# Kernel optimization log

Hardware: AMD Instinct MI355X
Metric: run time of the kernel (lower is better)

The kernel has to match this reference:

```python
import jax, jax.numpy as jnp
import numpy as np
from jax import lax

HIDDEN = 30
NUM_CLASSES = 10
SEQ = 784
BATCH = 16384


def setup_inputs() -> dict:
    key = jax.random.key(0)
    k = jax.random.split(key, 6)
    s_ih = 1.0  # fan_in = 1
    s_hh = 1.0 / np.sqrt(HIDDEN)
    s_lin = 1.0 / np.sqrt(HIDDEN)
    return {
        "inputs": jax.random.normal(k[0], (BATCH, SEQ), dtype=jnp.float32),
        "W_ih": jax.random.normal(k[1], (HIDDEN, 1), dtype=jnp.float32) * s_ih,
        "W_hh": jax.random.normal(k[2], (HIDDEN, HIDDEN), dtype=jnp.float32) * s_hh,
        "b_mod": jax.random.normal(k[3], (HIDDEN,), dtype=jnp.float32) * 0.1,
        "W_lin": jax.random.normal(k[4], (NUM_CLASSES, HIDDEN), dtype=jnp.float32) * s_lin,
        "b_lin": jax.random.normal(k[5], (NUM_CLASSES,), dtype=jnp.float32) * s_lin,
    }


def reference(inputs, W_ih, W_hh, b_mod, W_lin, b_lin):
    # inputs: [B, 784] pixel-by-pixel sequence. Scan over the 784 time steps.
    B = inputs.shape[0]
    # Precompute the input projection for all steps at once: [784, B, H]
    # (W_ih has shape [H, 1], so x_t @ W_ih.T == x_t[:, None] * W_ih[:, 0])
    x_proj = inputs.T[:, :, None] * W_ih[:, 0][None, None, :]  # [784, B, H]

    def step(h, xp):
        z = xp + h @ W_hh.T  # [B, H]
        # modReLU: sign(z) * relu(|z| + b)
        h_new = jnp.sign(z) * jax.nn.relu(jnp.abs(z) + b_mod)
        return h_new, None

    h0 = jnp.zeros((B, HIDDEN), dtype=inputs.dtype)
    h_final, _ = lax.scan(step, h0, x_proj)
    return h_final @ W_lin.T + b_lin  # [B, 10] logits
```

## Files before the change

kernel.cpp:

```cpp
#include <hip/hip_runtime.h>
#include <stdint.h>

#define HID 30
#define NCLS 10
#define SEQ 784
#define NBATCH 16384
#define TCH 112
#define NSTAGE 7
#define XPAD 116

typedef _Float16 f16x8 __attribute__((ext_vector_type(8)));
typedef _Float16 f16x2 __attribute__((ext_vector_type(2)));
typedef float f32x4 __attribute__((ext_vector_type(4)));
typedef uint32_t u32x4 __attribute__((ext_vector_type(4)));

static __device__ __forceinline__ f16x8 mkfrag16(uint32_t a, uint32_t b, uint32_t c, uint32_t d) {
    u32x4 t = {a, b, c, d};
    return __builtin_bit_cast(f16x8, t);
}

static __device__ __forceinline__ uint32_t pkf16(_Float16 lo, _Float16 hi) {
    return (uint32_t)__builtin_bit_cast(unsigned short, lo)
         | ((uint32_t)__builtin_bit_cast(unsigned short, hi) << 16);
}

static __device__ __forceinline__ uint32_t pk_rne(float a, float b) {
    return pkf16((_Float16)a, (_Float16)b);
}

static __device__ __forceinline__ uint32_t pkrtz(float a, float b) {
    return __builtin_bit_cast(uint32_t, __builtin_amdgcn_cvt_pkrtz(a, b));
}

static __device__ __forceinline__ uint32_t modrelu_pk(uint32_t z, uint32_t bp) {
    const f16x2 zero2 = {(_Float16)0.f, (_Float16)0.f};
    f16x2 t = __builtin_bit_cast(f16x2, z & 0x7FFF7FFFu) + __builtin_bit_cast(f16x2, bp);
    t = __builtin_elementwise_max(t, zero2);
    const uint32_t tb = __builtin_bit_cast(uint32_t, t);
    return (tb & 0x7FFF7FFFu) | (z & 0x80008000u);
}

static __device__ __forceinline__ uint32_t pkmax(uint32_t a, uint32_t b) {
    return __builtin_bit_cast(uint32_t,
        __builtin_elementwise_max(__builtin_bit_cast(f16x2, a), __builtin_bit_cast(f16x2, b)));
}

static __device__ __forceinline__ uint32_t scale_mul(uint32_t v, uint32_t sc32) {
    return __builtin_bit_cast(uint32_t,
        __builtin_bit_cast(f16x2, v) * __builtin_bit_cast(f16x2, sc32));
}

__launch_bounds__(64, 1)
__global__ void rnn_scan_kernel(const float* __restrict__ inp,
                                const float* __restrict__ W_ih,
                                const float* __restrict__ W_hh,
                                const float* __restrict__ b_mod,
                                const float* __restrict__ W_lin,
                                const float* __restrict__ b_lin,
                                float* __restrict__ out)
{
    __shared__ __align__(16) float xs_lds[16 * XPAD];

    const int lane = threadIdx.x;
    const int q = lane >> 4;
    const int n = lane & 15;
    const int b0 = blockIdx.x * 16;

    const int i1 = 8 * (n >> 2) + (n & 3);
    const int i2 = i1 + 4;

    uint32_t a1h[4], a1m[4], a2h[4], a2m[4];
    #pragma unroll
    for (int p = 0; p < 4; ++p) {
        _Float16 h1[2], m1[2], h2[2], m2[2];
        #pragma unroll
        for (int e = 0; e < 2; ++e) {
            const int j = 8 * q + 2 * p + e;
            float w1 = 0.f, w2 = 0.f;
            if (j < HID) {
                w1 = W_hh[i1 * HID + j];
                if (i2 < HID) w2 = W_hh[i2 * HID + j];
            } else if (j == HID) {
                w1 = W_ih[i1];
                if (i2 < HID) w2 = W_ih[i2];
            }
            h1[e] = (_Float16)w1; m1[e] = (_Float16)(w1 - (float)h1[e]);
            h2[e] = (_Float16)w2; m2[e] = (_Float16)(w2 - (float)h2[e]);
        }
        a1h[p] = pkf16(h1[0], h1[1]); a1m[p] = pkf16(m1[0], m1[1]);
        a2h[p] = pkf16(h2[0], h2[1]); a2m[p] = pkf16(m2[0], m2[1]);
    }
    const f16x8 A1h = mkfrag16(a1h[0], a1h[1], a1h[2], a1h[3]);
    const f16x8 A1m = mkfrag16(a1m[0], a1m[1], a1m[2], a1m[3]);
    const f16x8 A2h = mkfrag16(a2h[0], a2h[1], a2h[2], a2h[3]);
    const f16x8 A2m = mkfrag16(a2m[0], a2m[1], a2m[2], a2m[3]);

    uint32_t bSp[4];
    #pragma unroll
    for (int p = 0; p < 4; ++p) {
        const int ja = 8 * q + 2 * p;
        const int jb = ja + 1;
        const float ba = (ja < HID) ? b_mod[ja] : 0.f;
        const float bb = (jb < HID) ? b_mod[jb] : 0.f;
        bSp[p] = pk_rne(ba, bb);
    }

    uint32_t hp[4] = {0u, 0u, 0u, 0u};
    int xinv_e = 0;
    int pend_field = 15;

    const bool isq3 = (q == 3);
    const f32x4 z4 = {0.f, 0.f, 0.f, 0.f};

    auto do8 = [&](const uint32_t* xpk) {
        #pragma unroll
        for (int tt = 0; tt < 8; ++tt) {
            const f16x8 Bh = mkfrag16(hp[0], hp[1], hp[2], hp[3]);
            f32x4 d1 = __builtin_amdgcn_mfma_f32_16x16x32_f16(A1h, Bh, z4, 0, 0, 0);
            f32x4 d2 = __builtin_amdgcn_mfma_f32_16x16x32_f16(A2h, Bh, z4, 0, 0, 0);
            d1 = __builtin_amdgcn_mfma_f32_16x16x32_f16(A1m, Bh, d1, 0, 0, 0);
            d2 = __builtin_amdgcn_mfma_f32_16x16x32_f16(A2m, Bh, d2, 0, 0, 0);
            hp[0] = modrelu_pk(pk_rne(d1[0], d1[1]), bSp[0]);
            hp[1] = modrelu_pk(pk_rne(d1[2], d1[3]), bSp[1]);
            hp[2] = modrelu_pk(pk_rne(d2[0], d2[1]), bSp[2]);
            const uint32_t mr3 = modrelu_pk(pk_rne(d2[2], d2[3]), bSp[3]);
            hp[3] = isq3 ? xpk[(tt + 1) & 7] : mr3;
        }
    };

    for (int s = 0; s < NSTAGE; ++s) {
        #pragma unroll
        for (int r = 0; r < 7; ++r) {
            const int idx = r * 64 + lane;
            const int bl = idx / 28;
            const int t4 = idx % 28;
            const float4 v = *(const float4*)(inp + (size_t)(b0 + bl) * SEQ + s * TCH + t4 * 4);
            *(float4*)(&xs_lds[bl * XPAD + t4 * 4]) = v;
        }
        __syncthreads();

        const float* xrow = &xs_lds[n * XPAD];
        float4 xv0 = *(const float4*)(xrow);
        float4 xv1 = *(const float4*)(xrow + 4);

        for (int t16 = 0; t16 < 7; ++t16) {
            const uint32_t sc32 = (uint32_t)pend_field * 0x04000400u;
            #pragma unroll
            for (int p = 0; p < 4; ++p) hp[p] = scale_mul(hp[p], sc32);
            #pragma unroll
            for (int p = 0; p < 4; ++p) bSp[p] = scale_mul(bSp[p], sc32);
            xinv_e += pend_field - 15;

            const float fac = __uint_as_float((uint32_t)(127 + xinv_e) << 23);

            {
                const int toff = t16 * 16 + 8;
                const float4 xn0 = *(const float4*)(xrow + toff);
                const float4 xn1 = *(const float4*)(xrow + toff + 4);

                uint32_t xpk[8];
                xpk[0] = pkrtz(xv0.x * fac, 0.f); xpk[1] = pkrtz(xv0.y * fac, 0.f);
                xpk[2] = pkrtz(xv0.z * fac, 0.f); xpk[3] = pkrtz(xv0.w * fac, 0.f);
                xpk[4] = pkrtz(xv1.x * fac, 0.f); xpk[5] = pkrtz(xv1.y * fac, 0.f);
                xpk[6] = pkrtz(xv1.z * fac, 0.f); xpk[7] = pkrtz(xv1.w * fac, 0.f);
                hp[3] = isq3 ? xpk[0] : hp[3];

                {
                    uint32_t mx = pkmax(pkmax(hp[0] & 0x7FFF7FFFu, hp[1] & 0x7FFF7FFFu),
                                        pkmax(hp[2] & 0x7FFF7FFFu, hp[3] & 0x7FFF7FFFu));
                    mx = pkmax(mx, (uint32_t)__shfl_xor((int)mx, 16));
                    mx = pkmax(mx, (uint32_t)__shfl_xor((int)mx, 32));
                    const uint32_t e16 = max(mx & 0xFFFFu, mx >> 16);
                    const int e_raw = (int)(e16 >> 10);
                    pend_field = min(max(25 - e_raw, 1), 20);
                }

                do8(xpk);
                xv0 = xn0;
                xv1 = xn1;
            }

            {
                const int toff = (t16 < 6) ? (t16 + 1) * 16 : 0;
                const float4 xn0 = *(const float4*)(xrow + toff);
                const float4 xn1 = *(const float4*)(xrow + toff + 4);

                uint32_t xpk[8];
                xpk[0] = pkrtz(xv0.x * fac, 0.f); xpk[1] = pkrtz(xv0.y * fac, 0.f);
                xpk[2] = pkrtz(xv0.z * fac, 0.f); xpk[3] = pkrtz(xv0.w * fac, 0.f);
                xpk[4] = pkrtz(xv1.x * fac, 0.f); xpk[5] = pkrtz(xv1.y * fac, 0.f);
                xpk[6] = pkrtz(xv1.z * fac, 0.f); xpk[7] = pkrtz(xv1.w * fac, 0.f);
                hp[3] = isq3 ? xpk[0] : hp[3];

                do8(xpk);
                xv0 = xn0;
                xv1 = xn1;
            }
        }
        __syncthreads();
    }

    const float S = __uint_as_float((uint32_t)(127 - xinv_e) << 23);
    float hf[8];
    #pragma unroll
    for (int p = 0; p < 4; ++p) {
        const f16x2 v = __builtin_bit_cast(f16x2, hp[p]);
        hf[2 * p] = (float)v.x;
        hf[2 * p + 1] = (float)v.y;
    }
    float acc[NCLS];
    #pragma unroll
    for (int c = 0; c < NCLS; ++c) {
        float p = 0.f;
        #pragma unroll
        for (int k = 0; k < 8; ++k) {
            const int j = 8 * q + k;
            if (j < HID) p += W_lin[c * HID + j] * hf[k];
        }
        p += __shfl_xor(p, 16, 64);
        p += __shfl_xor(p, 32, 64);
        acc[c] = p * S + b_lin[c];
    }
    if (q == 0) {
        #pragma unroll
        for (int c = 0; c < NCLS; ++c)
            out[(size_t)(b0 + n) * NCLS + c] = acc[c];
    }
}

extern "C" void kernel_launch(void* const* d_in, const int* in_sizes, int n_in,
                              void* d_out, int out_size, void* d_ws, size_t ws_size,
                              hipStream_t stream) {
    const float* inp   = (const float*)d_in[0];
    const float* W_ih  = (const float*)d_in[1];
    const float* W_hh  = (const float*)d_in[2];
    const float* b_mod = (const float*)d_in[3];
    const float* W_lin = (const float*)d_in[4];
    const float* b_lin = (const float*)d_in[5];
    float* out = (float*)d_out;

    dim3 grid(NBATCH / 16);
    dim3 block(64);
    hipLaunchKernelGGL(rnn_scan_kernel, grid, block, 0, stream,
                       inp, W_ih, W_hh, b_mod, W_lin, b_lin, out);
}
```

Before: 181.8 us.

## Interleave two independent batch chains per wave and overlap exponent reductions

Each 64-thread block now carries two independent 16-sample recurrent chains (A and B). Their MFMA and modReLU steps are interleaved so one chain's dependent work can fill the other's MFMA latency. The cross-lane max shuffles used for dynamic rescaling are split and issued around the MFMA steps to hide their latency, and the grid is halved accordingly. The trade-off is twice the registers and LDS per block and only half as many waves, so some SIMDs may sit idle with 512 single-wave blocks.

```diff
diff --git a/kernel.cpp b/kernel.cpp
--- a/kernel.cpp
+++ b/kernel.cpp
@@ -20,8 +20,8 @@
 }
 
 static __device__ __forceinline__ uint32_t pkf16(_Float16 lo, _Float16 hi) {
-    return (uint32_t)__builtin_bit_cast(unsigned short, lo)
-         | ((uint32_t)__builtin_bit_cast(unsigned short, hi) << 16);
+    f16x2 v = {lo, hi};
+    return __builtin_bit_cast(uint32_t, v);
 }
 
 static __device__ __forceinline__ uint32_t pk_rne(float a, float b) {
@@ -59,12 +59,12 @@
                                 const float* __restrict__ b_lin,
                                 float* __restrict__ out)
 {
-    __shared__ __align__(16) float xs_lds[16 * XPAD];
+    __shared__ __align__(16) float xs_lds[32 * XPAD];
 
     const int lane = threadIdx.x;
     const int q = lane >> 4;
     const int n = lane & 15;
-    const int b0 = blockIdx.x * 16;
+    const int b0 = blockIdx.x * 32;
 
     const int i1 = 8 * (n >> 2) + (n & 3);
     const int i2 = i1 + 4;
@@ -95,42 +95,57 @@
     const f16x8 A2h = mkfrag16(a2h[0], a2h[1], a2h[2], a2h[3]);
     const f16x8 A2m = mkfrag16(a2m[0], a2m[1], a2m[2], a2m[3]);
 
-    uint32_t bSp[4];
+    uint32_t bSpA[4], bSpB[4];
     #pragma unroll
     for (int p = 0; p < 4; ++p) {
         const int ja = 8 * q + 2 * p;
         const int jb = ja + 1;
         const float ba = (ja < HID) ? b_mod[ja] : 0.f;
         const float bb = (jb < HID) ? b_mod[jb] : 0.f;
-        bSp[p] = pk_rne(ba, bb);
-    }
-
-    uint32_t hp[4] = {0u, 0u, 0u, 0u};
-    int xinv_e = 0;
-    int pend_field = 15;
+        const uint32_t v = pk_rne(ba, bb);
+        bSpA[p] = v;
+        bSpB[p] = v;
+    }
+
+    uint32_t hpA[4] = {0u, 0u, 0u, 0u};
+    uint32_t hpB[4] = {0u, 0u, 0u, 0u};
+    int xinvA = 0, xinvB = 0;
+    int pendA = 15, pendB = 15;
 
     const bool isq3 = (q == 3);
     const f32x4 z4 = {0.f, 0.f, 0.f, 0.f};
 
-    auto do8 = [&](const uint32_t* xpk) {
+    auto do8x2 = [&](const uint32_t* xa, const uint32_t* xb) {
         #pragma unroll
         for (int tt = 0; tt < 8; ++tt) {
-            const f16x8 Bh = mkfrag16(hp[0], hp[1], hp[2], hp[3]);
-            f32x4 d1 = __builtin_amdgcn_mfma_f32_16x16x32_f16(A1h, Bh, z4, 0, 0, 0);
-            f32x4 d2 = __builtin_amdgcn_mfma_f32_16x16x32_f16(A2h, Bh, z4, 0, 0, 0);
-            d1 = __builtin_amdgcn_mfma_f32_16x16x32_f16(A1m, Bh, d1, 0, 0, 0);
-            d2 = __builtin_amdgcn_mfma_f32_16x16x32_f16(A2m, Bh, d2, 0, 0, 0);
-            hp[0] = modrelu_pk(pk_rne(d1[0], d1[1]), bSp[0]);
-            hp[1] = modrelu_pk(pk_rne(d1[2], d1[3]), bSp[1]);
-            hp[2] = modrelu_pk(pk_rne(d2[0], d2[1]), bSp[2]);
-            const uint32_t mr3 = modrelu_pk(pk_rne(d2[2], d2[3]), bSp[3]);
-            hp[3] = isq3 ? xpk[(tt + 1) & 7] : mr3;
+            const f16x8 BA = mkfrag16(hpA[0], hpA[1], hpA[2], hpA[3]);
+            const f16x8 BB = mkfrag16(hpB[0], hpB[1], hpB[2], hpB[3]);
+            f32x4 d1A = __builtin_amdgcn_mfma_f32_16x16x32_f16(A1h, BA, z4, 0, 0, 0);
+            f32x4 d2A = __builtin_amdgcn_mfma_f32_16x16x32_f16(A2h, BA, z4, 0, 0, 0);
+            f32x4 d1B = __builtin_amdgcn_mfma_f32_16x16x32_f16(A1h, BB, z4, 0, 0, 0);
+            f32x4 d2B = __builtin_amdgcn_mfma_f32_16x16x32_f16(A2h, BB, z4, 0, 0, 0);
+            d1A = __builtin_amdgcn_mfma_f32_16x16x32_f16(A1m, BA, d1A, 0, 0, 0);
+            d2A = __builtin_amdgcn_mfma_f32_16x16x32_f16(A2m, BA, d2A, 0, 0, 0);
+            d1B = __builtin_amdgcn_mfma_f32_16x16x32_f16(A1m, BB, d1B, 0, 0, 0);
+            d2B = __builtin_amdgcn_mfma_f32_16x16x32_f16(A2m, BB, d2B, 0, 0, 0);
+
+            hpA[0] = modrelu_pk(pk_rne(d1A[0], d1A[1]), bSpA[0]);
+            hpA[1] = modrelu_pk(pk_rne(d1A[2], d1A[3]), bSpA[1]);
+            hpA[2] = modrelu_pk(pk_rne(d2A[0], d2A[1]), bSpA[2]);
+            const uint32_t mr3A = modrelu_pk(pk_rne(d2A[2], d2A[3]), bSpA[3]);
+            hpA[3] = isq3 ? xa[(tt + 1) & 7] : mr3A;
+
+            hpB[0] = modrelu_pk(pk_rne(d1B[0], d1B[1]), bSpB[0]);
+            hpB[1] = modrelu_pk(pk_rne(d1B[2], d1B[3]), bSpB[1]);
+            hpB[2] = modrelu_pk(pk_rne(d2B[0], d2B[1]), bSpB[2]);
+            const uint32_t mr3B = modrelu_pk(pk_rne(d2B[2], d2B[3]), bSpB[3]);
+            hpB[3] = isq3 ? xb[(tt + 1) & 7] : mr3B;
         }
     };
 
     for (int s = 0; s < NSTAGE; ++s) {
         #pragma unroll
-        for (int r = 0; r < 7; ++r) {
+        for (int r = 0; r < 14; ++r) {
             const int idx = r * 64 + lane;
             const int bl = idx / 28;
             const int t4 = idx % 28;
@@ -139,92 +154,133 @@
         }
         __syncthreads();
 
-        const float* xrow = &xs_lds[n * XPAD];
-        float4 xv0 = *(const float4*)(xrow);
-        float4 xv1 = *(const float4*)(xrow + 4);
+        const float* xrowA = &xs_lds[n * XPAD];
+        const float* xrowB = &xs_lds[(16 + n) * XPAD];
+        float4 xvA0 = *(const float4*)(xrowA);
+        float4 xvA1 = *(const float4*)(xrowA + 4);
+        float4 xvB0 = *(const float4*)(xrowB);
+        float4 xvB1 = *(const float4*)(xrowB + 4);
 
         for (int t16 = 0; t16 < 7; ++t16) {
-            const uint32_t sc32 = (uint32_t)pend_field * 0x04000400u;
+            const uint32_t scA = (uint32_t)pendA * 0x04000400u;
+            const uint32_t scB = (uint32_t)pendB * 0x04000400u;
             #pragma unroll
-            for (int p = 0; p < 4; ++p) hp[p] = scale_mul(hp[p], sc32);
+            for (int p = 0; p < 4; ++p) { hpA[p] = scale_mul(hpA[p], scA); hpB[p] = scale_mul(hpB[p], scB); }
             #pragma unroll
-            for (int p = 0; p < 4; ++p) bSp[p] = scale_mul(bSp[p], sc32);
-            xinv_e += pend_field - 15;
-
-            const float fac = __uint_as_float((uint32_t)(127 + xinv_e) << 23);
+            for (int p = 0; p < 4; ++p) { bSpA[p] = scale_mul(bSpA[p], scA); bSpB[p] = scale_mul(bSpB[p], scB); }
+            xinvA += pendA - 15;
+            xinvB += pendB - 15;
+
+            const float facA = __uint_as_float((uint32_t)(127 + xinvA) << 23);
+            const float facB = __uint_as_float((uint32_t)(127 + xinvB) << 23);
+
+            uint32_t mxA, mxB;
 
             {
                 const int toff = t16 * 16 + 8;
-                const float4 xn0 = *(const float4*)(xrow + toff);
-                const float4 xn1 = *(const float4*)(xrow + toff + 4);
-
-                uint32_t xpk[8];
-                xpk[0] = pkrtz(xv0.x * fac, 0.f); xpk[1] = pkrtz(xv0.y * fac, 0.f);
-                xpk[2] = pkrtz(xv0.z * fac, 0.f); xpk[3] = pkrtz(xv0.w * fac, 0.f);
-                xpk[4] = pkrtz(xv1.x * fac, 0.f); xpk[5] = pkrtz(xv1.y * fac, 0.f);
-                xpk[6] = pkrtz(xv1.z * fac, 0.f); xpk[7] = pkrtz(xv1.w * fac, 0.f);
-                hp[3] = isq3 ? xpk[0] : hp[3];
-
-                {
-                    uint32_t mx = pkmax(pkmax(hp[0] & 0x7FFF7FFFu, hp[1] & 0x7FFF7FFFu),
-                                        pkmax(hp[2] & 0x7FFF7FFFu, hp[3] & 0x7FFF7FFFu));
-                    mx = pkmax(mx, (uint32_t)__shfl_xor((int)mx, 16));
-                    mx = pkmax(mx, (uint32_t)__shfl_xor((int)mx, 32));
-                    const uint32_t e16 = max(mx & 0xFFFFu, mx >> 16);
-                    const int e_raw = (int)(e16 >> 10);
-                    pend_field = min(max(25 - e_raw, 1), 20);
-                }
-
-                do8(xpk);
-                xv0 = xn0;
-                xv1 = xn1;
+                const float4 xnA0 = *(const float4*)(xrowA + toff);
+                const float4 xnA1 = *(const float4*)(xrowA + toff + 4);
+                const float4 xnB0 = *(const float4*)(xrowB + toff);
+                const float4 xnB1 = *(const float4*)(xrowB + toff + 4);
+
+                uint32_t xa[8], xb[8];
+                xa[0] = pkrtz(xvA0.x * facA, 0.f); xa[1] = pkrtz(xvA0.y * facA, 0.f);
+                xa[2] = pkrtz(xvA0.z * facA, 0.f); xa[3] = pkrtz(xvA0.w * facA, 0.f);
+                xa[4] = pkrtz(xvA1.x * facA, 0.f); xa[5] = pkrtz(xvA1.y * facA, 0.f);
+                xa[6] = pkrtz(xvA1.z * facA, 0.f); xa[7] = pkrtz(xvA1.w * facA, 0.f);
+                xb[0] = pkrtz(xvB0.x * facB, 0.f); xb[1] = pkrtz(xvB0.y * facB, 0.f);
+                xb[2] = pkrtz(xvB0.z * facB, 0.f); xb[3] = pkrtz(xvB0.w * facB, 0.f);
+                xb[4] = pkrtz(xvB1.x * facB, 0.f); xb[5] = pkrtz(xvB1.y * facB, 0.f);
+                xb[6] = pkrtz(xvB1.z * facB, 0.f); xb[7] = pkrtz(xvB1.w * facB, 0.f);
+                hpA[3] = isq3 ? xa[0] : hpA[3];
+                hpB[3] = isq3 ? xb[0] : hpB[3];
+
+                mxA = pkmax(pkmax(hpA[0] & 0x7FFF7FFFu, hpA[1] & 0x7FFF7FFFu),
+                            pkmax(hpA[2] & 0x7FFF7FFFu, hpA[3] & 0x7FFF7FFFu));
+                mxB = pkmax(pkmax(hpB[0] & 0x7FFF7FFFu, hpB[1] & 0x7FFF7FFFu),
+                            pkmax(hpB[2] & 0x7FFF7FFFu, hpB[3] & 0x7FFF7FFFu));
+                const uint32_t shA1 = (uint32_t)__shfl_xor((int)mxA, 16);
+                const uint32_t shB1 = (uint32_t)__shfl_xor((int)mxB, 16);
+
+                do8x2(xa, xb);
+
+                mxA = pkmax(mxA, shA1);
+                mxB = pkmax(mxB, shB1);
+                xvA0 = xnA0; xvA1 = xnA1; xvB0 = xnB0; xvB1 = xnB1;
             }
+            const uint32_t shA2 = (uint32_t)__shfl_xor((int)mxA, 32);
+            const uint32_t shB2 = (uint32_t)__shfl_xor((int)mxB, 32);
 
             {
                 const int toff = (t16 < 6) ? (t16 + 1) * 16 : 0;
-                const float4 xn0 = *(const float4*)(xrow + toff);
-                const float4 xn1 = *(const float4*)(xrow + toff + 4);
-
-                uint32_t xpk[8];
-                xpk[0] = pkrtz(xv0.x * fac, 0.f); xpk[1] = pkrtz(xv0.y * fac, 0.f);
-                xpk[2] = pkrtz(xv0.z * fac, 0.f); xpk[3] = pkrtz(xv0.w * fac, 0.f);
-                xpk[4] = pkrtz(xv1.x * fac, 0.f); xpk[5] = pkrtz(xv1.y * fac, 0.f);
-                xpk[6] = pkrtz(xv1.z * fac, 0.f); xpk[7] = pkrtz(xv1.w * fac, 0.f);
-                hp[3] = isq3 ? xpk[0] : hp[3];
-
-                do8(xpk);
-                xv0 = xn0;
-                xv1 = xn1;
+                const float4 xnA0 = *(const float4*)(xrowA + toff);
+                const float4 xnA1 = *(const float4*)(xrowA + toff + 4);
+                const float4 xnB0 = *(const float4*)(xrowB + toff);
+                const float4 xnB1 = *(const float4*)(xrowB + toff + 4);
+
+                uint32_t xa[8], xb[8];
+                xa[0] = pkrtz(xvA0.x * facA, 0.f); xa[1] = pkrtz(xvA0.y * facA, 0.f);
+                xa[2] = pkrtz(xvA0.z * facA, 0.f); xa[3] = pkrtz(xvA0.w * facA, 0.f);
+                xa[4] = pkrtz(xvA1.x * facA, 0.f); xa[5] = pkrtz(xvA1.y * facA, 0.f);
+                xa[6] = pkrtz(xvA1.z * facA, 0.f); xa[7] = pkrtz(xvA1.w * facA, 0.f);
+                xb[0] = pkrtz(xvB0.x * facB, 0.f); xb[1] = pkrtz(xvB0.y * facB, 0.f);
+                xb[2] = pkrtz(xvB0.z * facB, 0.f); xb[3] = pkrtz(xvB0.w * facB, 0.f);
+                xb[4] = pkrtz(xvB1.x * facB, 0.f); xb[5] = pkrtz(xvB1.y * facB, 0.f);
+                xb[6] = pkrtz(xvB1.z * facB, 0.f); xb[7] = pkrtz(xvB1.w * facB, 0.f);
+                hpA[3] = isq3 ? xa[0] : hpA[3];
+                hpB[3] = isq3 ? xb[0] : hpB[3];
+
+                do8x2(xa, xb);
+
+                xvA0 = xnA0; xvA1 = xnA1; xvB0 = xnB0; xvB1 = xnB1;
             }
+
+            mxA = pkmax(mxA, shA2);
+            mxB = pkmax(mxB, shB2);
+            const uint32_t eA = max(mxA & 0xFFFFu, mxA >> 16);
+            const uint32_t eB = max(mxB & 0xFFFFu, mxB >> 16);
+            pendA = min(max(25 - (int)(eA >> 10), 1), 20);
+            pendB = min(max(25 - (int)(eB >> 10), 1), 20);
         }
         __syncthreads();
     }
 
-    const float S = __uint_as_float((uint32_t)(127 - xinv_e) << 23);
-    float hf[8];
+    const float SA = __uint_as_float((uint32_t)(127 - xinvA) << 23);
+    const float SB = __uint_as_float((uint32_t)(127 - xinvB) << 23);
+    float hfA[8], hfB[8];
     #pragma unroll
     for (int p = 0; p < 4; ++p) {
-        const f16x2 v = __builtin_bit_cast(f16x2, hp[p]);
-        hf[2 * p] = (float)v.x;
-        hf[2 * p + 1] = (float)v.y;
-    }
-    float acc[NCLS];
+        const f16x2 va = __builtin_bit_cast(f16x2, hpA[p]);
+        const f16x2 vb = __builtin_bit_cast(f16x2, hpB[p]);
+        hfA[2 * p] = (float)va.x; hfA[2 * p + 1] = (float)va.y;
+        hfB[2 * p] = (float)vb.x; hfB[2 * p + 1] = (float)vb.y;
+    }
+    float accA[NCLS], accB[NCLS];
     #pragma unroll
     for (int c = 0; c < NCLS; ++c) {
-        float p = 0.f;
+        float pA = 0.f, pB = 0.f;
         #pragma unroll
         for (int k = 0; k < 8; ++k) {
             const int j = 8 * q + k;
-            if (j < HID) p += W_lin[c * HID + j] * hf[k];
-        }
-        p += __shfl_xor(p, 16, 64);
-        p += __shfl_xor(p, 32, 64);
-        acc[c] = p * S + b_lin[c];
+            if (j < HID) {
+                const float w = W_lin[c * HID + j];
+                pA += w * hfA[k];
+                pB += w * hfB[k];
+            }
+        }
+        pA += __shfl_xor(pA, 16, 64);
+        pA += __shfl_xor(pA, 32, 64);
+        pB += __shfl_xor(pB, 16, 64);
+        pB += __shfl_xor(pB, 32, 64);
+        accA[c] = pA * SA + b_lin[c];
+        accB[c] = pB * SB + b_lin[c];
     }
     if (q == 0) {
         #pragma unroll
-        for (int c = 0; c < NCLS; ++c)
-            out[(size_t)(b0 + n) * NCLS + c] = acc[c];
+        for (int c = 0; c < NCLS; ++c) {
+            out[(size_t)(b0 + n) * NCLS + c] = accA[c];
+            out[(size_t)(b0 + 16 + n) * NCLS + c] = accB[c];
+        }
     }
 }
 
@@ -239,7 +295,7 @@
     const float* b_lin = (const float*)d_in[5];
     float* out = (float*)d_out;
 
-    dim3 grid(NBATCH / 16);
+    dim3 grid(NBATCH / 32);
     dim3 block(64);
     hipLaunchKernelGGL(rnn_scan_kernel, grid, block, 0, stream,
                        inp, W_ih, W_hh, b_mod, W_lin, b_lin, out);
```

Measured after the change: 267.1 us. +46.9%, slower.
